# Kernel tuning notes

Hardware: AMD Instinct MI355X
Metric: run time of the kernel (lower is better)

The kernel has to match this reference:

```python
import jax, jax.numpy as jnp
import numpy as np

B, L = 4, 8192
IN_CH, OUT_CH = 1, 1
H = 64               # d_model
NSTATE = 16          # d_state
DBLK = 4             # number of residual blocks
DCONV = 16
EXPAND = 2
DINNER = EXPAND * H              # 128
HEADDIM = H // 4                 # 16
NHEADS = DINNER // HEADDIM       # 8
CONV_DIM = DINNER + 2 * NSTATE   # 160 (ngroups=1)
D_IN_PROJ = 2 * DINNER + 2 * NSTATE + NHEADS  # 296
CHUNK = 128


def setup_inputs():
    key = jax.random.key(0)
    ks = jax.random.split(key, 12)
    rn = lambda k, shape, s: (jax.random.normal(k, shape) * s).astype(jnp.float32)
    x = rn(ks[0], (B, L, IN_CH), 1.0)
    w_in = rn(ks[1], (H, IN_CH), 1.0)
    w_out = rn(ks[2], (OUT_CH, H), 1.0 / np.sqrt(H))
    in_proj_w = rn(ks[3], (DBLK, D_IN_PROJ, H), 1.0 / np.sqrt(H))
    conv_w = rn(ks[4], (DBLK, CONV_DIM, DCONV), 1.0 / np.sqrt(DCONV))
    conv_b = rn(ks[5], (DBLK, CONV_DIM), 0.02)
    dt = jnp.exp(jax.random.uniform(ks[6], (DBLK, NHEADS)) * (np.log(0.1) - np.log(1e-3)) + np.log(1e-3))
    dt_bias = (dt + jnp.log(-jnp.expm1(-dt))).astype(jnp.float32)  # inverse softplus
    A_log = jnp.log(jax.random.uniform(ks[7], (DBLK, NHEADS), minval=1.0, maxval=16.0)).astype(jnp.float32)
    D_skip = jnp.ones((DBLK, NHEADS), jnp.float32)
    init_states = rn(ks[8], (DBLK, NHEADS, HEADDIM, NSTATE), 0.01)
    norm_w = jnp.ones((DBLK, DINNER), jnp.float32)
    out_proj_w = rn(ks[9], (DBLK, H, DINNER), 1.0 / np.sqrt(DINNER))
    mlp_w = rn(ks[10], (DBLK, H, H), 1.0 / np.sqrt(H))
    mlp_b = jnp.zeros((DBLK, H), jnp.float32)
    return {"x": x, "w_in": w_in, "w_out": w_out, "in_proj_w": in_proj_w,
            "conv_w": conv_w, "conv_b": conv_b, "dt_bias": dt_bias, "A_log": A_log,
            "D_skip": D_skip, "init_states": init_states, "norm_w": norm_w,
            "out_proj_w": out_proj_w, "mlp_w": mlp_w, "mlp_b": mlp_b}


def segsum(a):
    # a: (..., q) -> (..., q, q); seg[i, j] = sum_{k=j+1..i} a[k] on lower triangle (diag=0), exp->0 above
    q = a.shape[-1]
    cs = jnp.cumsum(a, axis=-1)
    seg = cs[..., :, None] - cs[..., None, :]
    mask = jnp.tril(jnp.ones((q, q), dtype=bool))
    return jnp.where(mask, seg, -1e30)


def ssd(X, dA, Bm, Cm, init_state):
    # Chunked SSD (Mamba2 paper). X: (b,l,h,p) = x*dt, dA: (b,l,h), Bm/Cm: (b,l,n), init_state: (b,h,p,n)
    b, l, h, p = X.shape
    c = l // CHUNK
    X = X.reshape(b, c, CHUNK, h, p)
    Bm = Bm.reshape(b, c, CHUNK, NSTATE)
    Cm = Cm.reshape(b, c, CHUNK, NSTATE)
    A = dA.reshape(b, c, CHUNK, h).transpose(0, 3, 1, 2)  # (b,h,c,q)
    A_cs = jnp.cumsum(A, axis=-1)
    # intra-chunk (diagonal blocks)
    Lm = jnp.exp(segsum(A))  # (b,h,c,q,q)
    Y_diag = jnp.einsum('bcln,bcsn,bhcls,bcshp->bclhp', Cm, Bm, Lm, X)
    # per-chunk final states
    decay_states = jnp.exp(A_cs[..., -1:] - A_cs)  # (b,h,c,q)
    states = jnp.einsum('bcln,bhcl,bclhp->bchpn', Bm, decay_states, X)
    states = jnp.concatenate([init_state[:, None], states], axis=1)  # (b,c+1,h,p,n)
    # inter-chunk recurrence (vectorized via segsum over chunk decays)
    decay_chunk = jnp.exp(segsum(jnp.pad(A_cs[..., -1], ((0, 0), (0, 0), (1, 0)))))  # (b,h,c+1,c+1)
    new_states = jnp.einsum('bhzc,bchpn->bzhpn', decay_chunk, states)
    prev_states = new_states[:, :-1]  # state entering each chunk
    state_decay = jnp.exp(A_cs)
    Y_off = jnp.einsum('bcln,bchpn,bhcl->bclhp', Cm, prev_states, state_decay)
    return (Y_diag + Y_off).reshape(b, l, h, p)


def mamba2(u, w_inp, cw, cb, dtb, alog, dskip, istate, nw, w_outp):
    b, l, _ = u.shape
    zxbcdt = jnp.einsum('bld,ed->ble', u, w_inp)  # (b,l,296)
    z = zxbcdt[..., :DINNER]
    xBC = zxbcdt[..., DINNER:DINNER + CONV_DIM]
    dt = jax.nn.softplus(zxbcdt[..., DINNER + CONV_DIM:] + dtb)  # (b,l,h)
    # causal depthwise conv over seq + silu
    xBC = jax.lax.conv_general_dilated(
        xBC.transpose(0, 2, 1), cw[:, None, :], (1,), [(DCONV - 1, 0)],
        feature_group_count=CONV_DIM, dimension_numbers=('NCH', 'OIH', 'NCH'))
    xBC = jax.nn.silu(xBC + cb[None, :, None]).transpose(0, 2, 1)
    xs = xBC[..., :DINNER]
    Bm = xBC[..., DINNER:DINNER + NSTATE]
    Cm = xBC[..., DINNER + NSTATE:]
    A = -jnp.exp(alog)  # (h,)
    xh = xs.reshape(b, l, NHEADS, HEADDIM)
    init = jnp.broadcast_to(istate, (b,) + istate.shape)
    y = ssd(xh * dt[..., None], dt * A, Bm, Cm, init)
    y = y + xh * dskip[None, None, :, None]  # D skip
    y = y.reshape(b, l, DINNER)
    # gated RMSNorm: norm(y * silu(z)) * weight
    y = y * jax.nn.silu(z)
    y = y * jax.lax.rsqrt(jnp.mean(y * y, axis=-1, keepdims=True) + 1e-5) * nw
    return jnp.einsum('ble,de->bld', y, w_outp)


def reference(x, w_in, w_out, in_proj_w, conv_w, conv_b, dt_bias, A_log,
              D_skip, init_states, norm_w, out_proj_w, mlp_w, mlp_b):
    h = jnp.einsum('bli,hi->blh', x, w_in)
    for i in range(DBLK):
        y = mamba2(h, in_proj_w[i], conv_w[i], conv_b[i], dt_bias[i], A_log[i],
                   D_skip[i], init_states[i], norm_w[i], out_proj_w[i])
        t = y / jnp.sqrt(1.0 + y * y)  # TanhApprox
        y = jnp.einsum('blh,oh->blo', t, mlp_w[i]) + mlp_b[i]
        h = h + y  # residual
    return jnp.einsum('blh,oh->blo', h, w_out)
```

## Files before the change

### kernel.cpp

```cpp
#include <hip/hip_runtime.h>
#include <math.h>

#define NB 4
#define SEQ 8192
#define NT (NB*SEQ)
#define HDIM 64
#define NST 16
#define NBLK 4
#define KCONV 16
#define DIN 128
#define PDIM 16
#define NH 8
#define CDIM 160
#define EPROJ 296
#define CH 128
#define NC 64

typedef __attribute__((ext_vector_type(8))) short short8;
typedef __attribute__((ext_vector_type(4))) float f32x4;

__device__ __forceinline__ float sigf(float x){ return 1.0f/(1.0f+__expf(-x)); }

__device__ __forceinline__ unsigned short bf16r(float f){
  unsigned int u = __float_as_uint(f);
  u = (u + 0x7fffu + ((u >> 16) & 1u)) >> 16;
  return (unsigned short)u;
}
__device__ __forceinline__ unsigned int pk_bf16(float a, float b){
  return (unsigned int)bf16r(a) | ((unsigned int)bf16r(b) << 16);
}
__device__ __forceinline__ float bf16f(unsigned short h){
  return __uint_as_float(((unsigned int)h) << 16);
}

__global__ __launch_bounds__(256) void k_init(const float* __restrict__ x, const float* __restrict__ w_in,
                                              float* __restrict__ h,
                                              const float* __restrict__ w,
                                              unsigned short* __restrict__ whi,
                                              unsigned short* __restrict__ wlo){
  int bi = blockIdx.x;
  const int HB = (NT*HDIM)/256;
  if(bi < HB){
    int i = bi*256 + threadIdx.x;
    int t = i >> 6, d = i & 63;
    h[i] = x[t]*w_in[d];
  } else {
    int i = (bi - HB)*256 + threadIdx.x;
    if(i < NBLK*EPROJ*HDIM){
      float f = w[i];
      unsigned short hi = bf16r(f);
      float fh = bf16f(hi);
      whi[i] = hi;
      wlo[i] = bf16r(f - fh);
    }
  }
}

__global__ __launch_bounds__(1024) void k_front(const float* __restrict__ h,
                                                const unsigned short* __restrict__ whi,
                                                const unsigned short* __restrict__ wlo,
                                                const float* __restrict__ cw, const float* __restrict__ cb,
                                                const float* __restrict__ dtb, const float* __restrict__ alog,
                                                unsigned short* __restrict__ zxz,
                                                unsigned short* __restrict__ xbc,
                                                float* __restrict__ dt, float* __restrict__ acs,
                                                float* __restrict__ asum, float* __restrict__ S){
  __shared__ __align__(16) unsigned char smf[148480];
  unsigned short* Hh  = (unsigned short*)(smf);
  unsigned short* Hl  = (unsigned short*)(smf + 20736);
  float* zxcS         = (float*)(smf + 41472);
  unsigned short* XhT = (unsigned short*)(smf);
  unsigned short* XlT = (unsigned short*)(smf + 34816);
  unsigned short* BhT = (unsigned short*)(smf + 69632);
  unsigned short* BlT = (unsigned short*)(smf + 73984);
  float* dtraw = (float*)(smf + 136192);
  float* dtl   = (float*)(smf + 140288);
  float* wle   = (float*)(smf + 144384);

  int bc = blockIdx.x;
  int c = bc & 63, b = bc >> 6;
  int t0 = b*SEQ + c*CH;
  int tid = threadIdx.x, lane = tid & 63, wid = tid >> 6;
  int quad = lane >> 4, lq = lane & 15;

#pragma unroll
  for(int k=0;k<3;k++){
    int idx = tid + k*1024;
    if(idx < 2304){
      int tok = idx >> 4;
      int d0 = (idx & 15) * 4;
      float4 v;
      if(c == 0 && tok < 16){ v = make_float4(0.f,0.f,0.f,0.f); }
      else v = *(const float4*)(h + (size_t)(t0 - 16 + tok)*HDIM + d0);
      float vv[4] = {v.x, v.y, v.z, v.w};
      unsigned short hi4[4], lo4[4];
#pragma unroll
      for(int j=0;j<4;j++){
        unsigned short hi = bf16r(vv[j]);
        hi4[j] = hi;
        lo4[j] = bf16r(vv[j] - bf16f(hi));
      }
      uint2 ph, pl;
      ph.x = (unsigned int)hi4[0] | ((unsigned int)hi4[1] << 16);
      ph.y = (unsigned int)hi4[2] | ((unsigned int)hi4[3] << 16);
      pl.x = (unsigned int)lo4[0] | ((unsigned int)lo4[1] << 16);
      pl.y = (unsigned int)lo4[2] | ((unsigned int)lo4[3] << 16);
      *(uint2*)&Hh[tok*72 + d0] = ph;
      *(uint2*)&Hl[tok*72 + d0] = pl;
    }
  }
  __syncthreads();

  {
    int L = wid;
    int tg, et;
    if(L < 152){ tg = 1 + L/19; et = L % 19; } else { tg = 0; et = 8 + (L - 152); }
    {
      int e_a = et*16 + lq;
      int ec = (e_a < EPROJ) ? e_a : (EPROJ-1);
      const unsigned short* wh = whi + (size_t)ec*HDIM + quad*8;
      const unsigned short* wl = wlo + (size_t)ec*HDIM + quad*8;
      short8 ah0 = *(const short8*)wh;
      short8 ah1 = *(const short8*)(wh + 32);
      short8 al0 = *(const short8*)wl;
      short8 al1 = *(const short8*)(wl + 32);
      while(true){
        int Ln = L + 16;
        int tgn = 0, etn = 0;
        short8 nh0 = ah0, nh1 = ah1, nl0 = al0, nl1 = al1;
        if(Ln < 162){
          if(Ln < 152){ tgn = 1 + Ln/19; etn = Ln % 19; } else { tgn = 0; etn = 8 + (Ln - 152); }
          int e_n = etn*16 + lq;
          int ecn = (e_n < EPROJ) ? e_n : (EPROJ-1);
          const unsigned short* wh2 = whi + (size_t)ecn*HDIM + quad*8;
          const unsigned short* wl2 = wlo + (size_t)ecn*HDIM + quad*8;
          nh0 = *(const short8*)wh2;
          nh1 = *(const short8*)(wh2 + 32);
          nl0 = *(const short8*)wl2;
          nl1 = *(const short8*)(wl2 + 32);
        }
        const unsigned short* hrh = Hh + (tg*16 + lq)*72 + quad*8;
        const unsigned short* hrl = Hl + (tg*16 + lq)*72 + quad*8;
        short8 xh0 = *(const short8*)hrh;
        short8 xh1 = *(const short8*)(hrh + 32);
        short8 xl0 = *(const short8*)hrl;
        short8 xl1 = *(const short8*)(hrl + 32);
        f32x4 acc = {0.f,0.f,0.f,0.f};
        acc = __builtin_amdgcn_mfma_f32_16x16x32_bf16(ah0, xh0, acc, 0, 0, 0);
        acc = __builtin_amdgcn_mfma_f32_16x16x32_bf16(ah1, xh1, acc, 0, 0, 0);
        acc = __builtin_amdgcn_mfma_f32_16x16x32_bf16(ah0, xl0, acc, 0, 0, 0);
        acc = __builtin_amdgcn_mfma_f32_16x16x32_bf16(ah1, xl1, acc, 0, 0, 0);
        acc = __builtin_amdgcn_mfma_f32_16x16x32_bf16(al0, xh0, acc, 0, 0, 0);
        acc = __builtin_amdgcn_mfma_f32_16x16x32_bf16(al1, xh1, acc, 0, 0, 0);
        if(tg >= 1){
          int tokg = t0 + (tg-1)*16 + lq;
#pragma unroll
          for(int r=0;r<4;r++){
            int e = et*16 + quad*4 + r;
            if(e < 128)        zxz[(size_t)e*NT + tokg] = bf16r(acc[r]);
            else if(e < 288)   zxcS[(e-128)*148 + tg*16 + lq] = acc[r];
            else if(e < 296)   dtraw[(e-288)*128 + (tg-1)*16 + lq] = acc[r];
          }
        } else {
#pragma unroll
          for(int r=0;r<4;r++){
            int e = et*16 + quad*4 + r;
            zxcS[(e-128)*148 + lq] = acc[r];
          }
        }
        if(Ln >= 162) break;
        L = Ln; tg = tgn; et = etn;
        ah0 = nh0; ah1 = nh1; al0 = nl0; al1 = nl1;
      }
    }
  }
  __syncthreads();

  unsigned int hiP[3][4], loP[3][4];
#pragma unroll
  for(int it=0; it<3; it++){
    int G = tid + it*1024;
    if(G < 2560){
      int ch = G >> 4, sg = (G & 15)*8;
      float buf[24];
#pragma unroll
      for(int q4=0;q4<6;q4++){
        float4 f = *(const float4*)&zxcS[ch*148 + sg + q4*4];
        buf[q4*4+0]=f.x; buf[q4*4+1]=f.y; buf[q4*4+2]=f.z; buf[q4*4+3]=f.w;
      }
      float wv[16];
#pragma unroll
      for(int k=0;k<16;k++) wv[k] = cw[ch*KCONV + k];
      float bias = cb[ch];
      unsigned short hs[8], ls[8];
#pragma unroll
      for(int s=0;s<8;s++){
        float acc = bias;
#pragma unroll
        for(int k=0;k<16;k++) acc += wv[k]*buf[s+1+k];
        float r = acc * sigf(acc);
        unsigned short hi = bf16r(r);
        hs[s] = hi;
        ls[s] = bf16r(r - bf16f(hi));
      }
      hiP[it][0] = (unsigned int)hs[0] | ((unsigned int)hs[1] << 16);
      hiP[it][1] = (unsigned int)hs[2] | ((unsigned int)hs[3] << 16);
      hiP[it][2] = (unsigned int)hs[4] | ((unsigned int)hs[5] << 16);
      hiP[it][3] = (unsigned int)hs[6] | ((unsigned int)hs[7] << 16);
      loP[it][0] = (unsigned int)ls[0] | ((unsigned int)ls[1] << 16);
      loP[it][1] = (unsigned int)ls[2] | ((unsigned int)ls[3] << 16);
      loP[it][2] = (unsigned int)ls[4] | ((unsigned int)ls[5] << 16);
      loP[it][3] = (unsigned int)ls[6] | ((unsigned int)ls[7] << 16);
      uint4 pk;
      pk.x = hiP[it][0]; pk.y = hiP[it][1]; pk.z = hiP[it][2]; pk.w = hiP[it][3];
      *(uint4*)(xbc + (size_t)ch*NT + t0 + sg) = pk;
    }
  }
  {
    int hh = tid >> 7, s = tid & 127;
    float raw = dtraw[hh*128 + s] + dtb[hh];
    float v = (raw > 20.f) ? raw : log1pf(__expf(raw));
    dtl[hh*128 + s] = v;
    dt[(size_t)hh*NT + t0 + s] = v;
  }
  __syncthreads();

#pragma unroll
  for(int it=0; it<3; it++){
    int G = tid + it*1024;
    if(G < 2560){
      int ch = G >> 4, sg = (G & 15)*8;
      if(ch < 128){
        uint4 vh; vh.x=hiP[it][0]; vh.y=hiP[it][1]; vh.z=hiP[it][2]; vh.w=hiP[it][3];
        uint4 vl; vl.x=loP[it][0]; vl.y=loP[it][1]; vl.z=loP[it][2]; vl.w=loP[it][3];
        *(uint4*)&XhT[ch*136 + sg] = vh;
        *(uint4*)&XlT[ch*136 + sg] = vl;
      } else if(ch < 144){
        uint4 vh; vh.x=hiP[it][0]; vh.y=hiP[it][1]; vh.z=hiP[it][2]; vh.w=hiP[it][3];
        uint4 vl; vl.x=loP[it][0]; vl.y=loP[it][1]; vl.z=loP[it][2]; vl.w=loP[it][3];
        *(uint4*)&BhT[(ch-128)*136 + sg] = vh;
        *(uint4*)&BlT[(ch-128)*136 + sg] = vl;
      }
    }
  }
  if(wid < 8){
    int hh = wid;
    float A = -__expf(alog[hh]);
    float2 dd = *(const float2*)&dtl[hh*128 + 2*lane];
    float d0 = dd.x, d1 = dd.y;
    float v0 = d0*A, v1 = d1*A;
    float s = v0 + v1;
    for(int off=1; off<64; off<<=1){
      float o = __shfl_up(s, off);
      if(lane >= off) s += o;
    }
    float tot = __shfl(s, 63);
    float excl = s - (v0+v1);
    float a0 = excl+v0, a1 = excl+v0+v1;
    *(float2*)&acs[(size_t)hh*NT + t0 + 2*lane] = make_float2(a0, a1);
    if(lane == 63) asum[(size_t)bc*NH + hh] = __expf(tot);
    wle[hh*128 + 2*lane]   = d0*__expf(tot - a0);
    wle[hh*128 + 2*lane+1] = d1*__expf(tot - a1);
  }
  __syncthreads();

  if(wid < 8){
    int hh = wid;
    f32x4 acc = {0.f,0.f,0.f,0.f};
#pragma unroll
    for(int kb=0;kb<4;kb++){
      int k0 = kb*32 + quad*8;
      short8 xh = *(const short8*)&XhT[(hh*16 + lq)*136 + k0];
      short8 xl = *(const short8*)&XlT[(hh*16 + lq)*136 + k0];
      float4 w0 = *(const float4*)&wle[hh*128 + k0];
      float4 w1 = *(const float4*)&wle[hh*128 + k0 + 4];
      float wv8[8] = {w0.x,w0.y,w0.z,w0.w,w1.x,w1.y,w1.z,w1.w};
      short8 ah, al;
#pragma unroll
      for(int j=0;j<8;j++){
        float xv = bf16f((unsigned short)xh[j]) + bf16f((unsigned short)xl[j]);
        float pw = xv * wv8[j];
        unsigned short hi = bf16r(pw);
        ah[j] = (short)hi;
        al[j] = (short)bf16r(pw - bf16f(hi));
      }
      short8 bh = *(const short8*)&BhT[lq*136 + k0];
      short8 bl = *(const short8*)&BlT[lq*136 + k0];
      acc = __builtin_amdgcn_mfma_f32_16x16x32_bf16(ah, bh, acc, 0, 0, 0);
      acc = __builtin_amdgcn_mfma_f32_16x16x32_bf16(ah, bl, acc, 0, 0, 0);
      acc = __builtin_amdgcn_mfma_f32_16x16x32_bf16(al, bh, acc, 0, 0, 0);
    }
    float* Sp = S + ((size_t)bc*NH + hh)*256;
#pragma unroll
    for(int r=0;r<4;r++) Sp[(quad*4 + r)*16 + lq] = acc[r];
  }
}

__global__ __launch_bounds__(64) void k_scan(const float* __restrict__ S, const float* __restrict__ easum,
                                             const float* __restrict__ init, float* __restrict__ prev){
  int q  = blockIdx.x & 3;
  int hh = (blockIdx.x >> 2) & 7;
  int b  = blockIdx.x >> 5;
  int el = q*64 + threadIdx.x;
  const size_t cs = (size_t)NH*256;
  const float* Sp = S + ((size_t)(b*NC)*NH + hh)*256 + el;
  float* Pp = prev + ((size_t)(b*NC)*NH + hh)*256 + el;
  const float* ap = easum + (size_t)(b*NC)*NH + hh;
  float e[NC];
#pragma unroll
  for(int c=0;c<NC;c++) e[c] = ap[(size_t)c*NH];
  float r = init[hh*256 + el];
  float s0 = Sp[0], s1 = Sp[cs], s2 = Sp[2*cs], s3 = Sp[3*cs];
#pragma unroll
  for(int c=0;c<NC;c+=4){
    Pp[(size_t)c*cs] = r;
    r = e[c]*r + s0;
    s0 = (c+4 < NC) ? Sp[(size_t)(c+4)*cs] : 0.f;
    Pp[(size_t)(c+1)*cs] = r;
    r = e[c+1]*r + s1;
    s1 = (c+5 < NC) ? Sp[(size_t)(c+5)*cs] : 0.f;
    Pp[(size_t)(c+2)*cs] = r;
    r = e[c+2]*r + s2;
    s2 = (c+6 < NC) ? Sp[(size_t)(c+6)*cs] : 0.f;
    Pp[(size_t)(c+3)*cs] = r;
    r = e[c+3]*r + s3;
    s3 = (c+7 < NC) ? Sp[(size_t)(c+7)*cs] : 0.f;
  }
}

__global__ __launch_bounds__(1024) void k_tail(const unsigned short* __restrict__ xbc,
                                               const unsigned short* __restrict__ zxz,
                                               const float* __restrict__ dt, const float* __restrict__ acs,
                                               const float* __restrict__ prev, const float* __restrict__ dskip,
                                               const float* __restrict__ nw, const float* __restrict__ opw,
                                               const float* __restrict__ mw, const float* __restrict__ mb,
                                               float* __restrict__ h,
                                               int last, const float* __restrict__ wout,
                                               float* __restrict__ out){
  __shared__ __align__(16) unsigned char sm[151840];
  unsigned short* Bb   = (unsigned short*)(sm);
  unsigned short* Cb   = (unsigned short*)(sm + 6144);
  unsigned short* XbT  = (unsigned short*)(sm + 12288);
  unsigned short* P0   = (unsigned short*)(sm + 55296);
  unsigned short* P1   = (unsigned short*)(sm + 98304);
  float* Al  = (float*)(sm + 141312);
  float* Dtl = (float*)(sm + 145408);
  float* nwl = (float*)(sm + 149504);
  float* mbl = (float*)(sm + 150016);
  unsigned short* zbuf = (unsigned short*)(sm + 150272);
  float* ssl  = (float*)(sm + 150304);
  float* outb = (float*)(sm + 151328);
  unsigned short* Zb = XbT;
  unsigned short* Wo = P0;
  unsigned short* Wm = P0 + 64*136;
  unsigned short* Yn = P1;
  unsigned short* Tt = P1;

  int bc = blockIdx.x;
  int c = bc & 63, b = bc >> 6;
  int t0 = b*SEQ + c*CH;
  int tid = threadIdx.x, lane = tid & 63, wid = tid >> 6;
  int quad = lane >> 4, lq = lane & 15;
  int hgrp = wid >> 3;
  int wr7 = wid & 7;
  int widr = (wr7 < 4) ? wr7 : (11 - wr7);
  int strip = widr*16;

#pragma unroll
  for(int k=0;k<4;k++){
    int idx = tid + k*1024;
    int ch = idx >> 7, s = idx & 127;
    unsigned short f = xbc[(size_t)(DIN+ch)*NT + t0 + s];
    if(ch < 16) Bb[s*24 + ch] = f;
    else        Cb[s*24 + ch-16] = f;
  }
#pragma unroll
  for(int k=0;k<4;k++){
    int fi = tid + k*1024;
    int p = fi >> 5, s4 = fi & 31;
    uint2 xu = *(const uint2*)&xbc[(size_t)p*NT + t0 + s4*4];
    float4 dv = *(const float4*)&dt[(size_t)(p>>4)*NT + t0 + s4*4];
    float x0 = bf16f((unsigned short)(xu.x & 0xffffu));
    float x1 = bf16f((unsigned short)(xu.x >> 16));
    float x2 = bf16f((unsigned short)(xu.y & 0xffffu));
    float x3 = bf16f((unsigned short)(xu.y >> 16));
    *(unsigned int*)&XbT[p*168 + s4*4]   = pk_bf16(x0*dv.x, x1*dv.y);
    *(unsigned int*)&XbT[p*168 + s4*4+2] = pk_bf16(x2*dv.z, x3*dv.w);
  }
#pragma unroll
  for(int k=0;k<2;k++){
    int idx = tid + k*1024;
    int hh = idx >> 8, rest = idx & 255;
    int p = rest >> 4, n = rest & 15;
    XbT[(hh*16+p)*168 + 128 + n] = bf16r(prev[((size_t)bc*NH + hh)*256 + rest]);
  }
#pragma unroll
  for(int k=0;k<2;k++){
    int idx = tid + k*1024;
    if(idx < 1536){
      int p = idx / 12, cc = idx - p*12;
      *(unsigned int*)&XbT[p*168 + 144 + 2*cc] = 0u;
    }
  }
  {
    int hh = tid >> 7, s = tid & 127;
    Al[hh*128+s]  = acs[(size_t)hh*NT + t0 + s];
    Dtl[hh*128+s] = dt[(size_t)hh*NT + t0 + s];
  }
  if(tid < 128) nwl[tid] = nw[tid];
  else if(tid < 192) mbl[tid-128] = mb[tid-128];
  else if(tid < 208) zbuf[tid-192] = 0;
  {
    unsigned short* Pgz = hgrp ? P1 : P0;
#pragma unroll
    for(int k=0;k<3;k++){
      int idx = lane + k*64;
      int rr = idx / 12, cc = idx - rr*12;
      *(unsigned int*)&Pgz[(strip+rr)*168 + 144 + 2*cc] = 0u;
    }
    int zc0 = (widr+1)*16;
    int nu  = (7 - widr)*8;
    for(int u = lane>>4; u < nu; u += 4){
      *(unsigned int*)&Pgz[(strip+(lane&15))*168 + zc0 + 2*u] = 0u;
    }
  }
  __syncthreads();

  short8 afr;
  {
    int row = strip + lq;
    const unsigned short* ap = (quad < 2) ? &Cb[row*24 + quad*8] : zbuf;
    afr = *(const short8*)ap;
  }
  f32x4 sc[8];
#pragma unroll
  for(int nt=0;nt<8;nt++){
    f32x4 acc = {0.f,0.f,0.f,0.f};
    if(nt <= widr){
      const unsigned short* bp = (quad < 2) ? &Bb[(nt*16+lq)*24 + quad*8] : zbuf;
      short8 bfr = *(const short8*)bp;
      acc = __builtin_amdgcn_mfma_f32_16x16x32_bf16(afr, bfr, acc, 0, 0, 0);
    }
    sc[nt] = acc;
  }

  unsigned short* Pg = hgrp ? P1 : P0;
  f32x4 accv[4];
  for(int j=0;j<4;j++){
    int hh2 = hgrp*4 + j;
    const float* Alh = Al + hh2*128;
    float alr[4];
#pragma unroll
    for(int r=0;r<4;r++) alr[r] = Alh[strip + quad*4 + r];
#pragma unroll
    for(int nt=0;nt<8;nt++){
      if(nt <= widr){
        int col = nt*16 + lq;
        float alc = Alh[col];
#pragma unroll
        for(int r=0;r<4;r++){
          int row = strip + quad*4 + r;
          float p = sc[nt][r] * __expf(alr[r] - alc);
          p = (col <= row) ? p : 0.f;
          Pg[row*168 + col] = bf16r(p);
        }
      }
    }
    {
      int n = lane & 15, rg = lane >> 4;
#pragma unroll
      for(int rr=0;rr<4;rr++){
        int row = strip + rg*4 + rr;
        float ea = __expf(Alh[row]);
        Pg[row*168 + 128 + n] = bf16r(bf16f(Cb[row*24+n]) * ea);
      }
    }
    f32x4 acc2 = {0.f,0.f,0.f,0.f};
#pragma unroll
    for(int ks=0;ks<5;ks++){
      short8 bfr = *(const short8*)&XbT[(hh2*16+lq)*168 + ks*32 + quad*8];
      short8 af  = *(const short8*)&Pg[(strip+lq)*168 + ks*32 + quad*8];
      acc2 = __builtin_amdgcn_mfma_f32_16x16x32_bf16(af, bfr, acc2, 0, 0, 0);
    }
    const float* Dth = Dtl + hh2*128;
    float Dk = dskip[hh2];
#pragma unroll
    for(int r=0;r<4;r++){
      int l = strip + quad*4 + r;
      float xdt = bf16f(XbT[(hh2*16+lq)*168 + l]);
      float dtv = fmaxf(Dth[l], 1e-30f);
      acc2[r] += Dk * xdt * __frcp_rn(dtv);
    }
    accv[j] = acc2;
  }
  __syncthreads();

#pragma unroll
  for(int k=0;k<4;k++){
    int fi = tid + k*1024;
    int p = fi >> 5, s4 = fi & 31;
    uint2 zu = *(const uint2*)&zxz[(size_t)p*NT + t0 + s4*4];
    *(unsigned int*)&Zb[p*136 + s4*4]   = zu.x;
    *(unsigned int*)&Zb[p*136 + s4*4+2] = zu.y;
  }
#pragma unroll
  for(int k=0;k<2;k++){
    int fi = tid + k*1024;
    int n = fi >> 5, k4 = fi & 31;
    float4 wv = *(const float4*)&opw[(size_t)n*DIN + k4*4];
    *(unsigned int*)&Wo[n*136 + k4*4]   = pk_bf16(wv.x, wv.y);
    *(unsigned int*)&Wo[n*136 + k4*4+2] = pk_bf16(wv.z, wv.w);
  }
  {
    int fi = tid;
    int n = fi >> 4, k4 = fi & 15;
    float4 wv = *(const float4*)&mw[(size_t)n*HDIM + k4*4];
    *(unsigned int*)&Wm[n*72 + k4*4]   = pk_bf16(wv.x, wv.y);
    *(unsigned int*)&Wm[n*72 + k4*4+2] = pk_bf16(wv.z, wv.w);
  }
  __syncthreads();

  float part[4] = {0.f,0.f,0.f,0.f};
#pragma unroll
  for(int j=0;j<4;j++){
    int ch = (hgrp*4+j)*16 + lq;
    float nwv = nwl[ch];
#pragma unroll
    for(int r=0;r<4;r++){
      int l = strip + quad*4 + r;
      float zv = bf16f(Zb[ch*136 + l]);
      float g = zv * sigf(zv);
      float yv = accv[j][r] * g;
      part[r] += yv*yv;
      Yn[l*136 + ch] = bf16r(yv * nwv);
    }
  }
#pragma unroll
  for(int r=0;r<4;r++){
    part[r] += __shfl_xor(part[r],1); part[r] += __shfl_xor(part[r],2);
    part[r] += __shfl_xor(part[r],4); part[r] += __shfl_xor(part[r],8);
  }
  if(lq == 0){
#pragma unroll
    for(int r=0;r<4;r++) ssl[hgrp*128 + strip + quad*4 + r] = part[r];
  }
  __syncthreads();

  float rms_[4];
#pragma unroll
  for(int r=0;r<4;r++){
    int l = strip + quad*4 + r;
    rms_[r] = rsqrtf((ssl[l] + ssl[128+l])*(1.0f/128.0f) + 1e-5f);
  }
  short8 afk[4];
#pragma unroll
  for(int ks=0;ks<4;ks++) afk[ks] = *(const short8*)&Yn[(strip+lq)*136 + ks*32 + quad*8];
  f32x4 aco[2];
#pragma unroll
  for(int ntl=0;ntl<2;ntl++){ aco[ntl] = (f32x4){0.f,0.f,0.f,0.f}; }
#pragma unroll
  for(int ntl=0;ntl<2;ntl++){
    int nt = hgrp*2 + ntl;
#pragma unroll
    for(int ks=0;ks<4;ks++){
      short8 bfr = *(const short8*)&Wo[(nt*16+lq)*136 + ks*32 + quad*8];
      aco[ntl] = __builtin_amdgcn_mfma_f32_16x16x32_bf16(afk[ks], bfr, aco[ntl], 0, 0, 0);
    }
  }
  __syncthreads();
#pragma unroll
  for(int ntl=0;ntl<2;ntl++){
    int nt = hgrp*2 + ntl;
#pragma unroll
    for(int r=0;r<4;r++){
      int l = strip + quad*4 + r;
      float o = aco[ntl][r] * rms_[r];
      Tt[l*136 + nt*16+lq] = bf16r(o * rsqrtf(1.0f + o*o));
    }
  }
  __syncthreads();

  f32x4 acm[2];
#pragma unroll
  for(int ntl=0;ntl<2;ntl++){ acm[ntl] = (f32x4){0.f,0.f,0.f,0.f}; }
#pragma unroll
  for(int ks=0;ks<2;ks++){
    short8 af = *(const short8*)&Tt[(strip+lq)*136 + ks*32 + quad*8];
#pragma unroll
    for(int ntl=0;ntl<2;ntl++){
      int nt = hgrp*2 + ntl;
      short8 bfr = *(const short8*)&Wm[(nt*16+lq)*72 + ks*32 + quad*8];
      acm[ntl] = __builtin_amdgcn_mfma_f32_16x16x32_bf16(af, bfr, acm[ntl], 0, 0, 0);
    }
  }
  if(!last){
#pragma unroll
    for(int ntl=0;ntl<2;ntl++){
      int nt = hgrp*2 + ntl;
#pragma unroll
      for(int r=0;r<4;r++){
        int l = strip + quad*4 + r;
        int d = nt*16 + lq;
        size_t gi = (size_t)(t0+l)*HDIM + d;
        h[gi] += acm[ntl][r] + mbl[d];
      }
    }
  } else {
    float ps[4] = {0.f,0.f,0.f,0.f};
#pragma unroll
    for(int ntl=0;ntl<2;ntl++){
      int nt = hgrp*2 + ntl;
      int d = nt*16 + lq;
      float wo = wout[d];
      float bias = mbl[d];
#pragma unroll
      for(int r=0;r<4;r++){
        int l = strip + quad*4 + r;
        size_t gi = (size_t)(t0+l)*HDIM + d;
        float hn = h[gi] + acm[ntl][r] + bias;
        ps[r] += hn * wo;
      }
    }
#pragma unroll
    for(int r=0;r<4;r++){
      ps[r] += __shfl_xor(ps[r],1); ps[r] += __shfl_xor(ps[r],2);
      ps[r] += __shfl_xor(ps[r],4); ps[r] += __shfl_xor(ps[r],8);
    }
    if(hgrp == 1 && lq == 0){
#pragma unroll
      for(int r=0;r<4;r++) outb[strip + quad*4 + r] = ps[r];
    }
    __syncthreads();
    if(hgrp == 0 && lq == 0){
#pragma unroll
      for(int r=0;r<4;r++){
        int l = strip + quad*4 + r;
        out[t0 + l] = ps[r] + outb[l];
      }
    }
  }
}

extern "C" void kernel_launch(void* const* d_in, const int* in_sizes, int n_in,
                              void* d_out, int out_size, void* d_ws, size_t ws_size,
                              hipStream_t stream){
  const float* x          = (const float*)d_in[0];
  const float* w_in       = (const float*)d_in[1];
  const float* w_out      = (const float*)d_in[2];
  const float* in_proj_w  = (const float*)d_in[3];
  const float* conv_w     = (const float*)d_in[4];
  const float* conv_b     = (const float*)d_in[5];
  const float* dt_bias    = (const float*)d_in[6];
  const float* A_log      = (const float*)d_in[7];
  const float* D_skip     = (const float*)d_in[8];
  const float* init_st    = (const float*)d_in[9];
  const float* norm_w     = (const float*)d_in[10];
  const float* out_proj_w = (const float*)d_in[11];
  const float* mlp_w      = (const float*)d_in[12];
  const float* mlp_b      = (const float*)d_in[13];
  float* out = (float*)d_out;

  float* ws = (float*)d_ws;
  float* h    = ws; ws += (size_t)NT*HDIM;
  unsigned short* zxz = (unsigned short*)ws; ws += (size_t)(128*NT)/2;
  unsigned short* xbc = (unsigned short*)ws; ws += (size_t)(CDIM*NT)/2;
  float* dt   = ws; ws += (size_t)NH*NT;
  float* acs  = ws; ws += (size_t)NH*NT;
  float* asum = ws; ws += (size_t)NB*NC*NH;
  float* S    = ws; ws += (size_t)NB*NC*NH*256;
  float* prev = ws; ws += (size_t)NB*NC*NH*256;
  unsigned short* whi = (unsigned short*)ws; ws += (size_t)(NBLK*EPROJ*HDIM)/2;
  unsigned short* wlo = (unsigned short*)ws; ws += (size_t)(NBLK*EPROJ*HDIM)/2;

  k_init<<<(NT*HDIM)/256 + (NBLK*EPROJ*HDIM)/256, 256, 0, stream>>>(x, w_in, h, in_proj_w, whi, wlo);
  for(int i=0;i<NBLK;i++){
    k_front<<<NB*NC, 1024, 0, stream>>>(h, whi + (size_t)i*EPROJ*HDIM, wlo + (size_t)i*EPROJ*HDIM,
                                        conv_w + i*CDIM*KCONV, conv_b + i*CDIM,
                                        dt_bias + i*NH, A_log + i*NH,
                                        zxz, xbc, dt, acs, asum, S);
    k_scan  <<<NB*NH*4, 64, 0, stream>>>(S, asum, init_st + i*NH*256, prev);
    k_tail  <<<NB*NC, 1024, 0, stream>>>(xbc, zxz, dt, acs, prev, D_skip + i*NH,
                                         norm_w + i*DIN, out_proj_w + i*HDIM*DIN,
                                         mlp_w + i*HDIM*HDIM, mlp_b + i*HDIM, h,
                                         (i == NBLK-1) ? 1 : 0, w_out, out);
  }
}
```

Before: 329.7 us.

## Fuse front, scan and tail into one cooperative kernel per layer

```diff
diff --git a/kernel.cpp b/kernel.cpp
--- a/kernel.cpp
+++ b/kernel.cpp
@@ -1,5 +1,8 @@
 #include <hip/hip_runtime.h>
+#include <hip/hip_cooperative_groups.h>
 #include <math.h>
+
+namespace cg = cooperative_groups;
 
 #define NB 4
 #define SEQ 8192
@@ -56,32 +59,55 @@
   }
 }
 
-__global__ __launch_bounds__(1024) void k_front(const float* __restrict__ h,
-                                                const unsigned short* __restrict__ whi,
-                                                const unsigned short* __restrict__ wlo,
-                                                const float* __restrict__ cw, const float* __restrict__ cb,
-                                                const float* __restrict__ dtb, const float* __restrict__ alog,
-                                                unsigned short* __restrict__ zxz,
-                                                unsigned short* __restrict__ xbc,
-                                                float* __restrict__ dt, float* __restrict__ acs,
-                                                float* __restrict__ asum, float* __restrict__ S){
-  __shared__ __align__(16) unsigned char smf[148480];
-  unsigned short* Hh  = (unsigned short*)(smf);
-  unsigned short* Hl  = (unsigned short*)(smf + 20736);
-  float* zxcS         = (float*)(smf + 41472);
-  unsigned short* XhT = (unsigned short*)(smf);
-  unsigned short* XlT = (unsigned short*)(smf + 34816);
-  unsigned short* BhT = (unsigned short*)(smf + 69632);
-  unsigned short* BlT = (unsigned short*)(smf + 73984);
-  float* dtraw = (float*)(smf + 136192);
-  float* dtl   = (float*)(smf + 140288);
-  float* wle   = (float*)(smf + 144384);
+__global__ __launch_bounds__(1024) void k_layer(
+    float* __restrict__ h,
+    const unsigned short* __restrict__ whi, const unsigned short* __restrict__ wlo,
+    const float* __restrict__ cw, const float* __restrict__ cb,
+    const float* __restrict__ dtb, const float* __restrict__ alog,
+    unsigned short* __restrict__ zxz,
+    float* __restrict__ S, float* __restrict__ easum, float* __restrict__ prev,
+    const float* __restrict__ initst,
+    const float* __restrict__ dskip, const float* __restrict__ nw,
+    const float* __restrict__ opw, const float* __restrict__ mw,
+    const float* __restrict__ mb,
+    int last, const float* __restrict__ wout, float* __restrict__ out){
+  __shared__ __align__(16) unsigned char sm[163104];
+  unsigned short* XbT = (unsigned short*)(sm);
+  unsigned short* Hh  = (unsigned short*)(sm);
+  unsigned short* Hl  = (unsigned short*)(sm + 20736);
+  unsigned short* Zb  = (unsigned short*)(sm);
+  float*          zxcS= (float*)(sm + 43008);
+  unsigned short* XhT = (unsigned short*)(sm + 43008);
+  unsigned short* XlT = (unsigned short*)(sm + 77824);
+  unsigned short* BhT = (unsigned short*)(sm + 112640);
+  unsigned short* BlT = (unsigned short*)(sm + 116992);
+  unsigned short* P0  = (unsigned short*)(sm + 43008);
+  unsigned short* P1  = (unsigned short*)(sm + 86016);
+  unsigned short* Wo  = (unsigned short*)(sm + 43008);
+  unsigned short* Wm  = (unsigned short*)(sm + 60416);
+  unsigned short* Yn  = P1;
+  unsigned short* Tt  = P1;
+  float* dtraw = (float*)(sm + 137728);
+  float* wle   = (float*)(sm + 137728);
+  float* ssl   = (float*)(sm + 137728);
+  float* outb  = (float*)(sm + 138752);
+  float* dtl   = (float*)(sm + 141824);
+  float* Al    = (float*)(sm + 145920);
+  unsigned short* Bb = (unsigned short*)(sm + 150016);
+  unsigned short* Cb = (unsigned short*)(sm + 156160);
+  float* nwl = (float*)(sm + 162304);
+  float* mbl = (float*)(sm + 162816);
+  unsigned short* zbuf = (unsigned short*)(sm + 163072);
 
   int bc = blockIdx.x;
   int c = bc & 63, b = bc >> 6;
   int t0 = b*SEQ + c*CH;
   int tid = threadIdx.x, lane = tid & 63, wid = tid >> 6;
   int quad = lane >> 4, lq = lane & 15;
+  int hgrp = wid >> 3;
+  int wr7 = wid & 7;
+  int widr = (wr7 < 4) ? wr7 : (11 - wr7);
+  int strip = widr*16;
 
 #pragma unroll
   for(int k=0;k<3;k++){
@@ -109,69 +135,70 @@
       *(uint2*)&Hl[tok*72 + d0] = pl;
     }
   }
+  if(tid < 128) nwl[tid] = nw[tid];
+  else if(tid < 192) mbl[tid-128] = mb[tid-128];
+  else if(tid < 208) zbuf[tid-192] = 0;
   __syncthreads();
 
   {
     int L = wid;
     int tg, et;
     if(L < 152){ tg = 1 + L/19; et = L % 19; } else { tg = 0; et = 8 + (L - 152); }
-    {
-      int e_a = et*16 + lq;
-      int ec = (e_a < EPROJ) ? e_a : (EPROJ-1);
-      const unsigned short* wh = whi + (size_t)ec*HDIM + quad*8;
-      const unsigned short* wl = wlo + (size_t)ec*HDIM + quad*8;
-      short8 ah0 = *(const short8*)wh;
-      short8 ah1 = *(const short8*)(wh + 32);
-      short8 al0 = *(const short8*)wl;
-      short8 al1 = *(const short8*)(wl + 32);
-      while(true){
-        int Ln = L + 16;
-        int tgn = 0, etn = 0;
-        short8 nh0 = ah0, nh1 = ah1, nl0 = al0, nl1 = al1;
-        if(Ln < 162){
-          if(Ln < 152){ tgn = 1 + Ln/19; etn = Ln % 19; } else { tgn = 0; etn = 8 + (Ln - 152); }
-          int e_n = etn*16 + lq;
-          int ecn = (e_n < EPROJ) ? e_n : (EPROJ-1);
-          const unsigned short* wh2 = whi + (size_t)ecn*HDIM + quad*8;
-          const unsigned short* wl2 = wlo + (size_t)ecn*HDIM + quad*8;
-          nh0 = *(const short8*)wh2;
-          nh1 = *(const short8*)(wh2 + 32);
-          nl0 = *(const short8*)wl2;
-          nl1 = *(const short8*)(wl2 + 32);
+    int e_a = et*16 + lq;
+    int ec = (e_a < EPROJ) ? e_a : (EPROJ-1);
+    const unsigned short* wh = whi + (size_t)ec*HDIM + quad*8;
+    const unsigned short* wl = wlo + (size_t)ec*HDIM + quad*8;
+    short8 ah0 = *(const short8*)wh;
+    short8 ah1 = *(const short8*)(wh + 32);
+    short8 al0 = *(const short8*)wl;
+    short8 al1 = *(const short8*)(wl + 32);
+    while(true){
+      int Ln = L + 16;
+      int tgn = 0, etn = 0;
+      short8 nh0 = ah0, nh1 = ah1, nl0 = al0, nl1 = al1;
+      if(Ln < 162){
+        if(Ln < 152){ tgn = 1 + Ln/19; etn = Ln % 19; } else { tgn = 0; etn = 8 + (Ln - 152); }
+        int e_n = etn*16 + lq;
+        int ecn = (e_n < EPROJ) ? e_n : (EPROJ-1);
+        const unsigned short* wh2 = whi + (size_t)ecn*HDIM + quad*8;
+        const unsigned short* wl2 = wlo + (size_t)ecn*HDIM + quad*8;
+        nh0 = *(const short8*)wh2;
+        nh1 = *(const short8*)(wh2 + 32);
+        nl0 = *(const short8*)wl2;
+        nl1 = *(const short8*)(wl2 + 32);
+      }
+      const unsigned short* hrh = Hh + (tg*16 + lq)*72 + quad*8;
+      const unsigned short* hrl = Hl + (tg*16 + lq)*72 + quad*8;
+      short8 xh0 = *(const short8*)hrh;
+      short8 xh1 = *(const short8*)(hrh + 32);
+      short8 xl0 = *(const short8*)hrl;
+      short8 xl1 = *(const short8*)(hrl + 32);
+      f32x4 acc = {0.f,0.f,0.f,0.f};
+      acc = __builtin_amdgcn_mfma_f32_16x16x32_bf16(ah0, xh0, acc, 0, 0, 0);
+      acc = __builtin_amdgcn_mfma_f32_16x16x32_bf16(ah1, xh1, acc, 0, 0, 0);
+      acc = __builtin_amdgcn_mfma_f32_16x16x32_bf16(ah0, xl0, acc, 0, 0, 0);
+      acc = __builtin_amdgcn_mfma_f32_16x16x32_bf16(ah1, xl1, acc, 0, 0, 0);
+      acc = __builtin_amdgcn_mfma_f32_16x16x32_bf16(al0, xh0, acc, 0, 0, 0);
+      acc = __builtin_amdgcn_mfma_f32_16x16x32_bf16(al1, xh1, acc, 0, 0, 0);
+      if(tg >= 1){
+        int tokg = t0 + (tg-1)*16 + lq;
+#pragma unroll
+        for(int r=0;r<4;r++){
+          int e = et*16 + quad*4 + r;
+          if(e < 128)        zxz[(size_t)e*NT + tokg] = bf16r(acc[r]);
+          else if(e < 288)   zxcS[(e-128)*148 + tg*16 + lq] = acc[r];
+          else if(e < 296)   dtraw[(e-288)*128 + (tg-1)*16 + lq] = acc[r];
         }
-        const unsigned short* hrh = Hh + (tg*16 + lq)*72 + quad*8;
-        const unsigned short* hrl = Hl + (tg*16 + lq)*72 + quad*8;
-        short8 xh0 = *(const short8*)hrh;
-        short8 xh1 = *(const short8*)(hrh + 32);
-        short8 xl0 = *(const short8*)hrl;
-        short8 xl1 = *(const short8*)(hrl + 32);
-        f32x4 acc = {0.f,0.f,0.f,0.f};
-        acc = __builtin_amdgcn_mfma_f32_16x16x32_bf16(ah0, xh0, acc, 0, 0, 0);
-        acc = __builtin_amdgcn_mfma_f32_16x16x32_bf16(ah1, xh1, acc, 0, 0, 0);
-        acc = __builtin_amdgcn_mfma_f32_16x16x32_bf16(ah0, xl0, acc, 0, 0, 0);
-        acc = __builtin_amdgcn_mfma_f32_16x16x32_bf16(ah1, xl1, acc, 0, 0, 0);
-        acc = __builtin_amdgcn_mfma_f32_16x16x32_bf16(al0, xh0, acc, 0, 0, 0);
-        acc = __builtin_amdgcn_mfma_f32_16x16x32_bf16(al1, xh1, acc, 0, 0, 0);
-        if(tg >= 1){
-          int tokg = t0 + (tg-1)*16 + lq;
-#pragma unroll
-          for(int r=0;r<4;r++){
-            int e = et*16 + quad*4 + r;
-            if(e < 128)        zxz[(size_t)e*NT + tokg] = bf16r(acc[r]);
-            else if(e < 288)   zxcS[(e-128)*148 + tg*16 + lq] = acc[r];
-            else if(e < 296)   dtraw[(e-288)*128 + (tg-1)*16 + lq] = acc[r];
-          }
-        } else {
-#pragma unroll
-          for(int r=0;r<4;r++){
-            int e = et*16 + quad*4 + r;
-            zxcS[(e-128)*148 + lq] = acc[r];
-          }
+      } else {
+#pragma unroll
+        for(int r=0;r<4;r++){
+          int e = et*16 + quad*4 + r;
+          zxcS[(e-128)*148 + lq] = acc[r];
         }
-        if(Ln >= 162) break;
-        L = Ln; tg = tgn; et = etn;
-        ah0 = nh0; ah1 = nh1; al0 = nl0; al1 = nl1;
-      }
+      }
+      if(Ln >= 162) break;
+      L = Ln; tg = tgn; et = etn;
+      ah0 = nh0; ah1 = nh1; al0 = nl0; al1 = nl1;
     }
   }
   __syncthreads();
@@ -211,9 +238,6 @@
       loP[it][1] = (unsigned int)ls[2] | ((unsigned int)ls[3] << 16);
       loP[it][2] = (unsigned int)ls[4] | ((unsigned int)ls[5] << 16);
       loP[it][3] = (unsigned int)ls[6] | ((unsigned int)ls[7] << 16);
-      uint4 pk;
-      pk.x = hiP[it][0]; pk.y = hiP[it][1]; pk.z = hiP[it][2]; pk.w = hiP[it][3];
-      *(uint4*)(xbc + (size_t)ch*NT + t0 + sg) = pk;
     }
   }
   {
@@ -221,7 +245,6 @@
     float raw = dtraw[hh*128 + s] + dtb[hh];
     float v = (raw > 20.f) ? raw : log1pf(__expf(raw));
     dtl[hh*128 + s] = v;
-    dt[(size_t)hh*NT + t0 + s] = v;
   }
   __syncthreads();
 
@@ -230,17 +253,44 @@
     int G = tid + it*1024;
     if(G < 2560){
       int ch = G >> 4, sg = (G & 15)*8;
+      uint4 vh; vh.x=hiP[it][0]; vh.y=hiP[it][1]; vh.z=hiP[it][2]; vh.w=hiP[it][3];
+      uint4 vl; vl.x=loP[it][0]; vl.y=loP[it][1]; vl.z=loP[it][2]; vl.w=loP[it][3];
       if(ch < 128){
-        uint4 vh; vh.x=hiP[it][0]; vh.y=hiP[it][1]; vh.z=hiP[it][2]; vh.w=hiP[it][3];
-        uint4 vl; vl.x=loP[it][0]; vl.y=loP[it][1]; vl.z=loP[it][2]; vl.w=loP[it][3];
         *(uint4*)&XhT[ch*136 + sg] = vh;
         *(uint4*)&XlT[ch*136 + sg] = vl;
+        const float* dtp = dtl + (ch>>4)*128 + sg;
+#pragma unroll
+        for(int s2=0;s2<4;s2++){
+          unsigned int u = hiP[it][s2];
+          float x0 = bf16f((unsigned short)(u & 0xffffu));
+          float x1 = bf16f((unsigned short)(u >> 16));
+          *(unsigned int*)&XbT[ch*168 + sg + 2*s2] = pk_bf16(x0*dtp[2*s2], x1*dtp[2*s2+1]);
+        }
       } else if(ch < 144){
-        uint4 vh; vh.x=hiP[it][0]; vh.y=hiP[it][1]; vh.z=hiP[it][2]; vh.w=hiP[it][3];
-        uint4 vl; vl.x=loP[it][0]; vl.y=loP[it][1]; vl.z=loP[it][2]; vl.w=loP[it][3];
         *(uint4*)&BhT[(ch-128)*136 + sg] = vh;
         *(uint4*)&BlT[(ch-128)*136 + sg] = vl;
-      }
+#pragma unroll
+        for(int s2=0;s2<4;s2++){
+          unsigned int u = hiP[it][s2];
+          Bb[(sg+2*s2)*24 + (ch-128)]   = (unsigned short)(u & 0xffffu);
+          Bb[(sg+2*s2+1)*24 + (ch-128)] = (unsigned short)(u >> 16);
+        }
+      } else {
+#pragma unroll
+        for(int s2=0;s2<4;s2++){
+          unsigned int u = hiP[it][s2];
+          Cb[(sg+2*s2)*24 + (ch-144)]   = (unsigned short)(u & 0xffffu);
+          Cb[(sg+2*s2+1)*24 + (ch-144)] = (unsigned short)(u >> 16);
+        }
+      }
+    }
+  }
+#pragma unroll
+  for(int k=0;k<2;k++){
+    int idx = tid + k*1024;
+    if(idx < 1536){
+      int p = idx / 12, cc = idx - p*12;
+      *(unsigned int*)&XbT[p*168 + 144 + 2*cc] = 0u;
     }
   }
   if(wid < 8){
@@ -257,8 +307,9 @@
     float tot = __shfl(s, 63);
     float excl = s - (v0+v1);
     float a0 = excl+v0, a1 = excl+v0+v1;
-    *(float2*)&acs[(size_t)hh*NT + t0 + 2*lane] = make_float2(a0, a1);
-    if(lane == 63) asum[(size_t)bc*NH + hh] = __expf(tot);
+    Al[hh*128 + 2*lane] = a0;
+    Al[hh*128 + 2*lane + 1] = a1;
+    if(lane == 63) easum[(size_t)bc*NH + hh] = __expf(tot);
     wle[hh*128 + 2*lane]   = d0*__expf(tot - a0);
     wle[hh*128 + 2*lane+1] = d1*__expf(tot - a1);
   }
@@ -294,99 +345,56 @@
 #pragma unroll
     for(int r=0;r<4;r++) Sp[(quad*4 + r)*16 + lq] = acc[r];
   }
-}
-
-__global__ __launch_bounds__(64) void k_scan(const float* __restrict__ S, const float* __restrict__ easum,
-                                             const float* __restrict__ init, float* __restrict__ prev){
-  int q  = blockIdx.x & 3;
-  int hh = (blockIdx.x >> 2) & 7;
-  int b  = blockIdx.x >> 5;
-  int el = q*64 + threadIdx.x;
-  const size_t cs = (size_t)NH*256;
-  const float* Sp = S + ((size_t)(b*NC)*NH + hh)*256 + el;
-  float* Pp = prev + ((size_t)(b*NC)*NH + hh)*256 + el;
-  const float* ap = easum + (size_t)(b*NC)*NH + hh;
-  float e[NC];
-#pragma unroll
-  for(int c=0;c<NC;c++) e[c] = ap[(size_t)c*NH];
-  float r = init[hh*256 + el];
-  float s0 = Sp[0], s1 = Sp[cs], s2 = Sp[2*cs], s3 = Sp[3*cs];
-#pragma unroll
-  for(int c=0;c<NC;c+=4){
-    Pp[(size_t)c*cs] = r;
-    r = e[c]*r + s0;
-    s0 = (c+4 < NC) ? Sp[(size_t)(c+4)*cs] : 0.f;
-    Pp[(size_t)(c+1)*cs] = r;
-    r = e[c+1]*r + s1;
-    s1 = (c+5 < NC) ? Sp[(size_t)(c+5)*cs] : 0.f;
-    Pp[(size_t)(c+2)*cs] = r;
-    r = e[c+2]*r + s2;
-    s2 = (c+6 < NC) ? Sp[(size_t)(c+6)*cs] : 0.f;
-    Pp[(size_t)(c+3)*cs] = r;
-    r = e[c+3]*r + s3;
-    s3 = (c+7 < NC) ? Sp[(size_t)(c+7)*cs] : 0.f;
-  }
-}
-
-__global__ __launch_bounds__(1024) void k_tail(const unsigned short* __restrict__ xbc,
-                                               const unsigned short* __restrict__ zxz,
-                                               const float* __restrict__ dt, const float* __restrict__ acs,
-                                               const float* __restrict__ prev, const float* __restrict__ dskip,
-                                               const float* __restrict__ nw, const float* __restrict__ opw,
-                                               const float* __restrict__ mw, const float* __restrict__ mb,
-                                               float* __restrict__ h,
-                                               int last, const float* __restrict__ wout,
-                                               float* __restrict__ out){
-  __shared__ __align__(16) unsigned char sm[151840];
-  unsigned short* Bb   = (unsigned short*)(sm);
-  unsigned short* Cb   = (unsigned short*)(sm + 6144);
-  unsigned short* XbT  = (unsigned short*)(sm + 12288);
-  unsigned short* P0   = (unsigned short*)(sm + 55296);
-  unsigned short* P1   = (unsigned short*)(sm + 98304);
-  float* Al  = (float*)(sm + 141312);
-  float* Dtl = (float*)(sm + 145408);
-  float* nwl = (float*)(sm + 149504);
-  float* mbl = (float*)(sm + 150016);
-  unsigned short* zbuf = (unsigned short*)(sm + 150272);
-  float* ssl  = (float*)(sm + 150304);
-  float* outb = (float*)(sm + 151328);
-  unsigned short* Zb = XbT;
-  unsigned short* Wo = P0;
-  unsigned short* Wm = P0 + 64*136;
-  unsigned short* Yn = P1;
-  unsigned short* Tt = P1;
-
-  int bc = blockIdx.x;
-  int c = bc & 63, b = bc >> 6;
-  int t0 = b*SEQ + c*CH;
-  int tid = threadIdx.x, lane = tid & 63, wid = tid >> 6;
-  int quad = lane >> 4, lq = lane & 15;
-  int hgrp = wid >> 3;
-  int wr7 = wid & 7;
-  int widr = (wr7 < 4) ? wr7 : (11 - wr7);
-  int strip = widr*16;
-
-#pragma unroll
-  for(int k=0;k<4;k++){
-    int idx = tid + k*1024;
-    int ch = idx >> 7, s = idx & 127;
-    unsigned short f = xbc[(size_t)(DIN+ch)*NT + t0 + s];
-    if(ch < 16) Bb[s*24 + ch] = f;
-    else        Cb[s*24 + ch-16] = f;
-  }
-#pragma unroll
-  for(int k=0;k<4;k++){
-    int fi = tid + k*1024;
-    int p = fi >> 5, s4 = fi & 31;
-    uint2 xu = *(const uint2*)&xbc[(size_t)p*NT + t0 + s4*4];
-    float4 dv = *(const float4*)&dt[(size_t)(p>>4)*NT + t0 + s4*4];
-    float x0 = bf16f((unsigned short)(xu.x & 0xffffu));
-    float x1 = bf16f((unsigned short)(xu.x >> 16));
-    float x2 = bf16f((unsigned short)(xu.y & 0xffffu));
-    float x3 = bf16f((unsigned short)(xu.y >> 16));
-    *(unsigned int*)&XbT[p*168 + s4*4]   = pk_bf16(x0*dv.x, x1*dv.y);
-    *(unsigned int*)&XbT[p*168 + s4*4+2] = pk_bf16(x2*dv.z, x3*dv.w);
-  }
+  __syncthreads();
+
+  {
+    unsigned short* Pgz = hgrp ? P1 : P0;
+#pragma unroll
+    for(int k=0;k<3;k++){
+      int idx = lane + k*64;
+      int rr = idx / 12, cc = idx - rr*12;
+      *(unsigned int*)&Pgz[(strip+rr)*168 + 144 + 2*cc] = 0u;
+    }
+    int zc0 = (widr+1)*16;
+    int nu  = (7 - widr)*8;
+    for(int u = lane>>4; u < nu; u += 4){
+      *(unsigned int*)&Pgz[(strip+(lane&15))*168 + zc0 + 2*u] = 0u;
+    }
+  }
+  cg::this_grid().sync();
+
+  if(bc < 128 && tid < 64){
+    int q  = bc & 3;
+    int hh = (bc >> 2) & 7;
+    int b2 = bc >> 5;
+    int el = q*64 + tid;
+    const size_t cs = (size_t)NH*256;
+    const float* Sp = S + ((size_t)(b2*NC)*NH + hh)*256 + el;
+    float* Pp = prev + ((size_t)(b2*NC)*NH + hh)*256 + el;
+    const float* ap = easum + (size_t)(b2*NC)*NH + hh;
+    float e[NC];
+#pragma unroll
+    for(int cc=0;cc<NC;cc++) e[cc] = ap[(size_t)cc*NH];
+    float r = initst[hh*256 + el];
+    float s0 = Sp[0], s1 = Sp[cs], s2 = Sp[2*cs], s3 = Sp[3*cs];
+#pragma unroll
+    for(int cc=0;cc<NC;cc+=4){
+      Pp[(size_t)cc*cs] = r;
+      r = e[cc]*r + s0;
+      s0 = (cc+4 < NC) ? Sp[(size_t)(cc+4)*cs] : 0.f;
+      Pp[(size_t)(cc+1)*cs] = r;
+      r = e[cc+1]*r + s1;
+      s1 = (cc+5 < NC) ? Sp[(size_t)(cc+5)*cs] : 0.f;
+      Pp[(size_t)(cc+2)*cs] = r;
+      r = e[cc+2]*r + s2;
+      s2 = (cc+6 < NC) ? Sp[(size_t)(cc+6)*cs] : 0.f;
+      Pp[(size_t)(cc+3)*cs] = r;
+      r = e[cc+3]*r + s3;
+      s3 = (cc+7 < NC) ? Sp[(size_t)(cc+7)*cs] : 0.f;
+    }
+  }
+  cg::this_grid().sync();
+
 #pragma unroll
   for(int k=0;k<2;k++){
     int idx = tid + k*1024;
@@ -394,43 +402,13 @@
     int p = rest >> 4, n = rest & 15;
     XbT[(hh*16+p)*168 + 128 + n] = bf16r(prev[((size_t)bc*NH + hh)*256 + rest]);
   }
-#pragma unroll
-  for(int k=0;k<2;k++){
-    int idx = tid + k*1024;
-    if(idx < 1536){
-      int p = idx / 12, cc = idx - p*12;
-      *(unsigned int*)&XbT[p*168 + 144 + 2*cc] = 0u;
-    }
-  }
-  {
-    int hh = tid >> 7, s = tid & 127;
-    Al[hh*128+s]  = acs[(size_t)hh*NT + t0 + s];
-    Dtl[hh*128+s] = dt[(size_t)hh*NT + t0 + s];
-  }
-  if(tid < 128) nwl[tid] = nw[tid];
-  else if(tid < 192) mbl[tid-128] = mb[tid-128];
-  else if(tid < 208) zbuf[tid-192] = 0;
-  {
-    unsigned short* Pgz = hgrp ? P1 : P0;
-#pragma unroll
-    for(int k=0;k<3;k++){
-      int idx = lane + k*64;
-      int rr = idx / 12, cc = idx - rr*12;
-      *(unsigned int*)&Pgz[(strip+rr)*168 + 144 + 2*cc] = 0u;
-    }
-    int zc0 = (widr+1)*16;
-    int nu  = (7 - widr)*8;
-    for(int u = lane>>4; u < nu; u += 4){
-      *(unsigned int*)&Pgz[(strip+(lane&15))*168 + zc0 + 2*u] = 0u;
-    }
-  }
   __syncthreads();
 
   short8 afr;
   {
     int row = strip + lq;
-    const unsigned short* ap = (quad < 2) ? &Cb[row*24 + quad*8] : zbuf;
-    afr = *(const short8*)ap;
+    const unsigned short* ap2 = (quad < 2) ? &Cb[row*24 + quad*8] : zbuf;
+    afr = *(const short8*)ap2;
   }
   f32x4 sc[8];
 #pragma unroll
@@ -482,7 +460,7 @@
       short8 af  = *(const short8*)&Pg[(strip+lq)*168 + ks*32 + quad*8];
       acc2 = __builtin_amdgcn_mfma_f32_16x16x32_bf16(af, bfr, acc2, 0, 0, 0);
     }
-    const float* Dth = Dtl + hh2*128;
+    const float* Dth = dtl + hh2*128;
     float Dk = dskip[hh2];
 #pragma unroll
     for(int r=0;r<4;r++){
@@ -663,25 +641,34 @@
   float* ws = (float*)d_ws;
   float* h    = ws; ws += (size_t)NT*HDIM;
   unsigned short* zxz = (unsigned short*)ws; ws += (size_t)(128*NT)/2;
-  unsigned short* xbc = (unsigned short*)ws; ws += (size_t)(CDIM*NT)/2;
-  float* dt   = ws; ws += (size_t)NH*NT;
-  float* acs  = ws; ws += (size_t)NH*NT;
+  float* S    = ws; ws += (size_t)NB*NC*NH*256;
   float* asum = ws; ws += (size_t)NB*NC*NH;
-  float* S    = ws; ws += (size_t)NB*NC*NH*256;
   float* prev = ws; ws += (size_t)NB*NC*NH*256;
   unsigned short* whi = (unsigned short*)ws; ws += (size_t)(NBLK*EPROJ*HDIM)/2;
   unsigned short* wlo = (unsigned short*)ws; ws += (size_t)(NBLK*EPROJ*HDIM)/2;
 
   k_init<<<(NT*HDIM)/256 + (NBLK*EPROJ*HDIM)/256, 256, 0, stream>>>(x, w_in, h, in_proj_w, whi, wlo);
   for(int i=0;i<NBLK;i++){
-    k_front<<<NB*NC, 1024, 0, stream>>>(h, whi + (size_t)i*EPROJ*HDIM, wlo + (size_t)i*EPROJ*HDIM,
-                                        conv_w + i*CDIM*KCONV, conv_b + i*CDIM,
-                                        dt_bias + i*NH, A_log + i*NH,
-                                        zxz, xbc, dt, acs, asum, S);
-    k_scan  <<<NB*NH*4, 64, 0, stream>>>(S, asum, init_st + i*NH*256, prev);
-    k_tail  <<<NB*NC, 1024, 0, stream>>>(xbc, zxz, dt, acs, prev, D_skip + i*NH,
-                                         norm_w + i*DIN, out_proj_w + i*HDIM*DIN,
-                                         mlp_w + i*HDIM*HDIM, mlp_b + i*HDIM, h,
-                                         (i == NBLK-1) ? 1 : 0, w_out, out);
+    const unsigned short* whi_i = whi + (size_t)i*EPROJ*HDIM;
+    const unsigned short* wlo_i = wlo + (size_t)i*EPROJ*HDIM;
+    const float* cw_i   = conv_w + i*CDIM*KCONV;
+    const float* cb_i   = conv_b + i*CDIM;
+    const float* dtb_i  = dt_bias + i*NH;
+    const float* alog_i = A_log + i*NH;
+    const float* init_i = init_st + i*NH*256;
+    const float* dsk_i  = D_skip + i*NH;
+    const float* nw_i   = norm_w + i*DIN;
+    const float* opw_i  = out_proj_w + i*HDIM*DIN;
+    const float* mw_i   = mlp_w + i*HDIM*HDIM;
+    const float* mb_i   = mlp_b + i*HDIM;
+    int last = (i == NBLK-1) ? 1 : 0;
+    void* args[] = {
+      (void*)&h, (void*)&whi_i, (void*)&wlo_i, (void*)&cw_i, (void*)&cb_i,
+      (void*)&dtb_i, (void*)&alog_i, (void*)&zxz, (void*)&S, (void*)&asum,
+      (void*)&prev, (void*)&init_i, (void*)&dsk_i, (void*)&nw_i, (void*)&opw_i,
+      (void*)&mw_i, (void*)&mb_i, (void*)&last, (void*)&w_out, (void*)&out
+    };
+    hipLaunchCooperativeKernel((const void*)k_layer, dim3(NB*NC), dim3(1024),
+                               args, 0, stream);
   }
 }
```

Result: slower. 638.8 us (+93.8%).
